# Performance work log

Measured on AMD Instinct MI355X. Metric: run time of the kernel, lower is better.

Reference implementation:

```python
import jax, jax.numpy as jnp
import numpy as np

E, D, F = 32, 2048, 768  # num_experts, hidden_size, intermediate_size
B, S, TOPK = 2, 1024, 8
T = B * S


def setup_inputs() -> dict:
    key = jax.random.key(0)
    k1, k2, k3, k4, k5 = jax.random.split(key, 5)
    hidden_states = jax.random.normal(k1, (B, S, D), dtype=jnp.float32)
    routing_weights = jax.random.uniform(k2, (T, E), dtype=jnp.float32)
    router_indices = jax.random.randint(k3, (T, TOPK), 0, E)
    gate_up_proj = jax.random.normal(k4, (E, D, 2 * F), dtype=jnp.float32) * 0.02
    down_proj = jax.random.normal(k5, (E, F, D), dtype=jnp.float32) * 0.02
    return {
        "hidden_states": hidden_states,
        "routing_weights": routing_weights,
        "router_indices": router_indices,
        "gate_up_proj": gate_up_proj,
        "down_proj": down_proj,
    }


def reference(hidden_states, routing_weights, router_indices, gate_up_proj, down_proj):
    batch_size = hidden_states.shape[0]
    x = hidden_states.reshape(-1, D)  # (T, D)
    gate_up = jnp.einsum('TD,EDF->TEF', x, gate_up_proj)  # (T, E, 2F)
    gate, up = jnp.split(gate_up, 2, axis=-1)
    gated = up * jax.nn.silu(gate)  # (T, E, F)
    next_states = jnp.einsum('TEF,EFD->TED', gated, down_proj)  # (T, E, D)
    next_states = (next_states * routing_weights[..., None]).sum(axis=1)  # (T, D)
    return next_states.reshape(batch_size, -1, D)
```

## Files before the change

kernel.cpp:

```cpp
#include <hip/hip_runtime.h>
#include <stdint.h>

#define NE 32
#define ND 2048
#define NF 768
#define NF2 1536
#define NT 2048
#define NEF (NE * NF)
#define KH 12288

#define BM 128
#define BN 64
#define BK 32
#define BSTR 40

typedef __attribute__((ext_vector_type(8))) short short8;
typedef __attribute__((ext_vector_type(4))) float floatx4;

__device__ __forceinline__ unsigned pk_bf16(float a, float b) {
  union { float f; unsigned u; } ua, ub;
  ua.f = a; ub.f = b;
  unsigned ra = (ua.u + 0x7fffu + ((ua.u >> 16) & 1u)) >> 16;
  unsigned rb = (ub.u + 0x7fffu + ((ub.u >> 16) & 1u)) & 0xffff0000u;
  return ra | rb;
}
__device__ __forceinline__ unsigned short bf16_1(float a) {
  union { float f; unsigned u; } ua; ua.f = a;
  return (unsigned short)((ua.u + 0x7fffu + ((ua.u >> 16) & 1u)) >> 16);
}

#define GLOAD_LDS16(g, l)                                                     \
  __builtin_amdgcn_global_load_lds(                                           \
      (const __attribute__((address_space(1))) void*)(g),                     \
      (__attribute__((address_space(3))) void*)(l), 16, 0, 0)

#define MF(a, b, c) __builtin_amdgcn_mfma_f32_16x16x32_bf16(a, b, c, 0, 0, 0)

__global__ void k_cvt_x(const float* __restrict__ x, unsigned short* __restrict__ xb, int n4) {
  int i = blockIdx.x * blockDim.x + threadIdx.x;
  if (i < n4) {
    float4 v = ((const float4*)x)[i];
    uint2 o;
    o.x = pk_bf16(v.x, v.y);
    o.y = pk_bf16(v.z, v.w);
    ((uint2*)xb)[i] = o;
  }
}

template <int PAIR>
__global__ void k_trans(const float* __restrict__ in, unsigned short* __restrict__ out,
                        int R, int C, size_t zstride) {
  __shared__ float sT[64][65];
  in  += (size_t)blockIdx.z * zstride;
  out += (size_t)blockIdx.z * zstride;
  const int r0 = blockIdx.y * 64, c0 = blockIdx.x * 64;
  const int t = threadIdx.x;
  const int lrow = t >> 4, lc4 = (t & 15) * 4;
#pragma unroll
  for (int i = 0; i < 4; i++) {
    float4 v = *(const float4*)&in[(size_t)(r0 + lrow + i * 16) * C + c0 + lc4];
    sT[lrow + i * 16][lc4 + 0] = v.x;
    sT[lrow + i * 16][lc4 + 1] = v.y;
    sT[lrow + i * 16][lc4 + 2] = v.z;
    sT[lrow + i * 16][lc4 + 3] = v.w;
  }
  __syncthreads();
  const int c = t >> 2, rg = (t & 3) * 16;
  uint4 o0, o1;
  o0.x = pk_bf16(sT[rg + 0][c],  sT[rg + 1][c]);
  o0.y = pk_bf16(sT[rg + 2][c],  sT[rg + 3][c]);
  o0.z = pk_bf16(sT[rg + 4][c],  sT[rg + 5][c]);
  o0.w = pk_bf16(sT[rg + 6][c],  sT[rg + 7][c]);
  o1.x = pk_bf16(sT[rg + 8][c],  sT[rg + 9][c]);
  o1.y = pk_bf16(sT[rg + 10][c], sT[rg + 11][c]);
  o1.z = pk_bf16(sT[rg + 12][c], sT[rg + 13][c]);
  o1.w = pk_bf16(sT[rg + 14][c], sT[rg + 15][c]);
  int oc = c0 + c;
  if (PAIR) {
    oc = (oc < NF) ? (((oc >> 5) << 6) + (oc & 31))
                   : ((((oc - NF) >> 5) << 6) + 32 + ((oc - NF) & 31));
  }
  unsigned short* op = &out[(size_t)oc * R + r0 + rg];
  ((uint4*)op)[0] = o0;
  ((uint4*)op)[1] = o1;
}

__global__ __launch_bounds__(512, 2) void k_gemm1p(
    const unsigned short* __restrict__ xb,
    const unsigned short* __restrict__ w1t,
    const float* __restrict__ rw,
    unsigned short* __restrict__ gws)
{
  __shared__ unsigned short sA[2][2][8192];
  __shared__ unsigned short sB[2][2][8192];
  __shared__ float srw[256];

  const int bx = blockIdx.x;
  const int L  = (bx & 7) * 192 + (bx >> 3);
  const int e  = L / 48;
  const int rem = L - e * 48;
  const int mt = rem & 7, nt = rem >> 3;
  const int m0 = mt * 256, n0 = nt * 256;

  const int tid = threadIdx.x;
  const int wid = tid >> 6, lane = tid & 63;
  const int wm2 = wid >> 2, wn4 = wid & 3;
  const int l15 = lane & 15, qg = lane >> 4;
  const int hb = wn4 >> 1, rbB = (wn4 & 1) * 64;

  if (tid < 256) srw[tid] = rw[(size_t)(m0 + tid) * NE + e];

  const int aoff0 = l15 * 64 + ((qg * 8) ^ ((l15 & 7) << 3));
  const int aoff1 = l15 * 64 + (((32 + qg * 8)) ^ ((l15 & 7) << 3));

  const int r8 = tid >> 3;
  const int csrc = ((tid & 7) ^ (r8 & 7)) * 8;
  const unsigned short* w1e = w1t + (size_t)e * NF2 * ND;
  const unsigned short* aSrc = xb  + (size_t)(m0 + r8) * ND + csrc;
  const unsigned short* bSrc = w1e + (size_t)(n0 + r8) * ND + csrc;

#define STAGE_A(buf, h, kt) do {                                              \
    const unsigned short* _g = aSrc + (size_t)(h) * 128 * ND + (size_t)(kt) * 64; \
    GLOAD_LDS16(_g, &sA[buf][h][wid * 512]);                                  \
    GLOAD_LDS16(_g + (size_t)64 * ND, &sA[buf][h][wid * 512 + 4096]);         \
  } while (0)
#define STAGE_B(buf, h, kt) do {                                              \
    const unsigned short* _g = bSrc + (size_t)(h) * 128 * ND + (size_t)(kt) * 64; \
    GLOAD_LDS16(_g, &sB[buf][h][wid * 512]);                                  \
    GLOAD_LDS16(_g + (size_t)64 * ND, &sB[buf][h][wid * 512 + 4096]);         \
  } while (0)

#define DS_A(buf, q) {                                                        \
    a0s0 = *(const short8*)&sA[buf][wm2][((q) * 32 +  0) * 64 + aoff0];       \
    a0s1 = *(const short8*)&sA[buf][wm2][((q) * 32 +  0) * 64 + aoff1];       \
    a1s0 = *(const short8*)&sA[buf][wm2][((q) * 32 + 16) * 64 + aoff0];       \
    a1s1 = *(const short8*)&sA[buf][wm2][((q) * 32 + 16) * 64 + aoff1];       \
  }
#define DS_B(buf) {                                                           \
    b0s0 = *(const short8*)&sB[buf][hb][(rbB +  0) * 64 + aoff0];             \
    b0s1 = *(const short8*)&sB[buf][hb][(rbB +  0) * 64 + aoff1];             \
    b1s0 = *(const short8*)&sB[buf][hb][(rbB + 16) * 64 + aoff0];             \
    b1s1 = *(const short8*)&sB[buf][hb][(rbB + 16) * 64 + aoff1];             \
    b2s0 = *(const short8*)&sB[buf][hb][(rbB + 32) * 64 + aoff0];             \
    b2s1 = *(const short8*)&sB[buf][hb][(rbB + 32) * 64 + aoff1];             \
    b3s0 = *(const short8*)&sB[buf][hb][(rbB + 48) * 64 + aoff0];             \
    b3s1 = *(const short8*)&sB[buf][hb][(rbB + 48) * 64 + aoff1];             \
  }
#define MM(q) do {                                                            \
    __builtin_amdgcn_s_setprio(1);                                            \
    acc[(q)*2+0][0] = MF(a0s0, b0s0, acc[(q)*2+0][0]);                        \
    acc[(q)*2+0][0] = MF(a0s1, b0s1, acc[(q)*2+0][0]);                        \
    acc[(q)*2+0][1] = MF(a0s0, b1s0, acc[(q)*2+0][1]);                        \
    acc[(q)*2+0][1] = MF(a0s1, b1s1, acc[(q)*2+0][1]);                        \
    acc[(q)*2+0][2] = MF(a0s0, b2s0, acc[(q)*2+0][2]);                        \
    acc[(q)*2+0][2] = MF(a0s1, b2s1, acc[(q)*2+0][2]);                        \
    acc[(q)*2+0][3] = MF(a0s0, b3s0, acc[(q)*2+0][3]);                        \
    acc[(q)*2+0][3] = MF(a0s1, b3s1, acc[(q)*2+0][3]);                        \
    acc[(q)*2+1][0] = MF(a1s0, b0s0, acc[(q)*2+1][0]);                        \
    acc[(q)*2+1][0] = MF(a1s1, b0s1, acc[(q)*2+1][0]);                        \
    acc[(q)*2+1][1] = MF(a1s0, b1s0, acc[(q)*2+1][1]);                        \
    acc[(q)*2+1][1] = MF(a1s1, b1s1, acc[(q)*2+1][1]);                        \
    acc[(q)*2+1][2] = MF(a1s0, b2s0, acc[(q)*2+1][2]);                        \
    acc[(q)*2+1][2] = MF(a1s1, b2s1, acc[(q)*2+1][2]);                        \
    acc[(q)*2+1][3] = MF(a1s0, b3s0, acc[(q)*2+1][3]);                        \
    acc[(q)*2+1][3] = MF(a1s1, b3s1, acc[(q)*2+1][3]);                        \
    __builtin_amdgcn_s_setprio(0);                                            \
  } while (0)

#define BAR_OPEN  asm volatile("s_barrier" ::: "memory")
#define BAR_CLOSE asm volatile("s_waitcnt lgkmcnt(0)\n\ts_barrier" ::: "memory")
#define VM4 asm volatile("s_waitcnt vmcnt(4)" ::: "memory")
#define VM0 asm volatile("s_waitcnt vmcnt(0)" ::: "memory")
#define S23_ON(x) x
#define S23_OFF(x)

#define KITER(t1, t2, t3, S23, VMT)                                           \
  DS_A(0, 0) DS_B(0) STAGE_A(1, 0, t1); BAR_OPEN; MM(0); BAR_CLOSE;           \
  DS_A(0, 1) STAGE_A(1, 1, t1); BAR_OPEN; MM(1); BAR_CLOSE;                   \
  DS_A(0, 2) S23(STAGE_B(0, 0, t2);) BAR_OPEN; MM(2); BAR_CLOSE;              \
  DS_A(0, 3) S23(STAGE_B(0, 1, t2);) VMT; BAR_OPEN; MM(3); BAR_CLOSE;         \
  DS_A(1, 0) DS_B(1) S23(STAGE_A(0, 0, t2);) BAR_OPEN; MM(0); BAR_CLOSE;      \
  DS_A(1, 1) S23(STAGE_A(0, 1, t2);) BAR_OPEN; MM(1); BAR_CLOSE;              \
  DS_A(1, 2) S23(STAGE_B(1, 0, t3);) BAR_OPEN; MM(2); BAR_CLOSE;              \
  DS_A(1, 3) S23(STAGE_B(1, 1, t3);) VMT; BAR_OPEN; MM(3); BAR_CLOSE;

  short8 a0s0, a0s1, a1s0, a1s1;
  short8 b0s0, b0s1, b1s0, b1s1, b2s0, b2s1, b3s0, b3s1;
  floatx4 acc[8][4];
#pragma unroll
  for (int i = 0; i < 8; i++)
#pragma unroll
    for (int j = 0; j < 4; j++) acc[i][j] = (floatx4){0.f, 0.f, 0.f, 0.f};

  STAGE_B(0, 0, 0); STAGE_B(0, 1, 0);
  STAGE_A(0, 0, 0); STAGE_A(0, 1, 0);
  STAGE_B(1, 0, 1); STAGE_B(1, 1, 1);
  VM4; BAR_OPEN;

  const int nI = ND / 64 / 2;
  for (int i = 0; i < nI - 1; ++i) {
    const int t1 = 2 * i + 1, t2 = 2 * i + 2, t3 = 2 * i + 3;
    KITER(t1, t2, t3, S23_ON, VM4)
  }
  {
    const int t1 = ND / 64 - 1;
    KITER(t1, 0, 0, S23_OFF, VM0)
  }

  const size_t cb = (size_t)e * NF + (size_t)nt * 128 + wn4 * 32 + l15;
#pragma unroll
  for (int mf = 0; mf < 8; ++mf) {
    const int rbase = wm2 * 128 + mf * 16 + qg * 4;
#pragma unroll
    for (int nf = 0; nf < 2; ++nf)
#pragma unroll
      for (int r = 0; r < 4; ++r) {
        float g = acc[mf][nf][r];
        float u = acc[mf][nf + 2][r];
        float sig = __builtin_amdgcn_rcpf(1.f + __expf(-g));
        float val = u * g * sig * srw[rbase + r];
        gws[(size_t)(m0 + rbase + r) * NEF + cb + nf * 16] = bf16_1(val);
      }
  }
#undef STAGE_A
#undef STAGE_B
#undef DS_A
#undef DS_B
#undef MM
#undef KITER
}

__global__ __launch_bounds__(256, 3) void k_gemm1b(
    const unsigned short* __restrict__ xb,
    const unsigned short* __restrict__ w1t,
    const float* __restrict__ rw,
    unsigned short* __restrict__ gws,
    int e0)
{
  __shared__ unsigned short sA[BM * BK];
  __shared__ unsigned short sG[BN * BK];
  __shared__ unsigned short sU[BN * BK];
  __shared__ float srw[BM];

  const int el  = blockIdx.y;
  const int e   = e0 + el;
  const int mt  = blockIdx.x & 15;
  const int nt  = blockIdx.x >> 4;
  const int m0  = mt * BM, n0 = nt * BN;
  const int tid = threadIdx.x;
  const int wid = tid >> 6, lane = tid & 63;
  const int wm = wid >> 1, wn = wid & 1;
  const int l15 = lane & 15, q = lane >> 4;

  if (tid < BM) srw[tid] = rw[(size_t)(m0 + tid) * NE + e];

  floatx4 accG[4][2], accU[4][2];
#pragma unroll
  for (int i = 0; i < 4; i++)
#pragma unroll
    for (int j = 0; j < 2; j++) {
      accG[i][j] = (floatx4){0.f, 0.f, 0.f, 0.f};
      accU[i][j] = (floatx4){0.f, 0.f, 0.f, 0.f};
    }

  const unsigned short* w1e = w1t + (size_t)el * NF2 * ND;

  const int koff = (lane & 3) * 8;
  const unsigned short* aptr = xb + (size_t)(m0 + wid * 32 + (lane >> 2)) * ND + koff;
  unsigned short* aLds = &sA[wid * 32 * BK];
  const unsigned short* gptr = w1e + (size_t)(n0 + wid * 16 + (lane >> 2)) * ND + koff;
  const unsigned short* uptr = gptr + (size_t)NF * ND;
  unsigned short* gLds = &sG[wid * 16 * BK];
  unsigned short* uLds = &sU[wid * 16 * BK];

  for (int kb = 0; kb < ND / BK; ++kb) {
    __syncthreads();
    GLOAD_LDS16(aptr + kb * BK, aLds);
    GLOAD_LDS16(aptr + kb * BK + 16 * ND, aLds + 16 * BK);
    GLOAD_LDS16(gptr + kb * BK, gLds);
    GLOAD_LDS16(uptr + kb * BK, uLds);
    __syncthreads();

    short8 bg0 = *(const short8*)&sG[(wn * 32 + 0  + l15) * BK + q * 8];
    short8 bg1 = *(const short8*)&sG[(wn * 32 + 16 + l15) * BK + q * 8];
    short8 bu0 = *(const short8*)&sU[(wn * 32 + 0  + l15) * BK + q * 8];
    short8 bu1 = *(const short8*)&sU[(wn * 32 + 16 + l15) * BK + q * 8];
#pragma unroll
    for (int i = 0; i < 4; i++) {
      short8 af = *(const short8*)&sA[(wm * 64 + i * 16 + l15) * BK + q * 8];
      accG[i][0] = MF(af, bg0, accG[i][0]);
      accG[i][1] = MF(af, bg1, accG[i][1]);
      accU[i][0] = MF(af, bu0, accU[i][0]);
      accU[i][1] = MF(af, bu1, accU[i][1]);
    }
  }

  const size_t obase = (size_t)m0 * NEF + (size_t)e * NF + n0 + wn * 32;
#pragma unroll
  for (int i = 0; i < 4; i++)
#pragma unroll
    for (int j = 0; j < 2; j++)
#pragma unroll
      for (int r = 0; r < 4; r++) {
        int row = wm * 64 + i * 16 + q * 4 + r;
        float g = accG[i][j][r];
        float u = accU[i][j][r];
        float sig = __builtin_amdgcn_rcpf(1.f + __expf(-g));
        float val = u * g * sig * srw[row];
        gws[obase + (size_t)row * NEF + j * 16 + l15] = bf16_1(val);
      }
}

template<int KSTRIDE, int HITERS>
__global__ __launch_bounds__(256, 3) void k_gemm2b(
    const unsigned short* __restrict__ gb,
    const unsigned short* __restrict__ w2t,
    float* __restrict__ out,
    int kbase)
{
  __shared__ unsigned short sA[BM * BK];
  __shared__ unsigned short sB[BN * BK];

  const int mt = blockIdx.x & 15;
  const int nt = blockIdx.x >> 4;
  const int m0 = mt * BM, n0 = nt * BN;
  const int tid = threadIdx.x;
  const int wid = tid >> 6, lane = tid & 63;
  const int wm = wid >> 1, wn = wid & 1;
  const int l15 = lane & 15, q = lane >> 4;

  const int kb0 = blockIdx.y * HITERS;
  const int kb1 = kb0 + HITERS;

  floatx4 acc[4][2];
#pragma unroll
  for (int i = 0; i < 4; i++)
#pragma unroll
    for (int j = 0; j < 2; j++) acc[i][j] = (floatx4){0.f, 0.f, 0.f, 0.f};

  const int koff = (lane & 3) * 8;
  const unsigned short* aptr = gb + (size_t)(m0 + wid * 32 + (lane >> 2)) * NEF + kbase + koff;
  unsigned short* aLds = &sA[wid * 32 * BK];
  const unsigned short* bptr = w2t + (size_t)(n0 + wid * 16 + (lane >> 2)) * KSTRIDE + koff;
  unsigned short* bLds = &sB[wid * 16 * BK];

  for (int kb = kb0; kb < kb1; ++kb) {
    __syncthreads();
    GLOAD_LDS16(aptr + kb * BK, aLds);
    GLOAD_LDS16(aptr + kb * BK + 16 * NEF, aLds + 16 * BK);
    GLOAD_LDS16(bptr + kb * BK, bLds);
    __syncthreads();

    short8 b0 = *(const short8*)&sB[(wn * 32 + 0  + l15) * BK + q * 8];
    short8 b1 = *(const short8*)&sB[(wn * 32 + 16 + l15) * BK + q * 8];
#pragma unroll
    for (int i = 0; i < 4; i++) {
      short8 af = *(const short8*)&sA[(wm * 64 + i * 16 + l15) * BK + q * 8];
      acc[i][0] = MF(af, b0, acc[i][0]);
      acc[i][1] = MF(af, b1, acc[i][1]);
    }
  }

#pragma unroll
  for (int i = 0; i < 4; i++)
#pragma unroll
    for (int j = 0; j < 2; j++)
#pragma unroll
      for (int r = 0; r < 4; r++) {
        int row = wm * 64 + i * 16 + q * 4 + r;
        unsafeAtomicAdd(&out[(size_t)(m0 + row) * ND + n0 + wn * 32 + j * 16 + l15],
                        acc[i][j][r]);
      }
}

__global__ __launch_bounds__(256, 2) void k_gemm1_legacy(
    const unsigned short* __restrict__ xb, const float* __restrict__ w1,
    const float* __restrict__ rw, unsigned short* __restrict__ gws)
{
  __shared__ unsigned short sA[BM * BK];
  __shared__ unsigned short sG[BN * BSTR];
  __shared__ unsigned short sU[BN * BSTR];
  __shared__ float srw[BM];
  const int e = blockIdx.y, mt = blockIdx.x & 15, nt = blockIdx.x >> 4;
  const int m0 = mt * BM, n0 = nt * BN;
  const int tid = threadIdx.x, wid = tid >> 6, lane = tid & 63;
  const int wm = wid >> 1, wn = wid & 1, l15 = lane & 15, q = lane >> 4;
  if (tid < BM) srw[tid] = rw[(size_t)(m0 + tid) * NE + e];
  const float* w1e = w1 + (size_t)e * ND * (2 * NF);
  floatx4 accG[4][2], accU[4][2];
#pragma unroll
  for (int i = 0; i < 4; i++)
#pragma unroll
    for (int j = 0; j < 2; j++) {
      accG[i][j] = (floatx4){0.f, 0.f, 0.f, 0.f};
      accU[i][j] = (floatx4){0.f, 0.f, 0.f, 0.f};
    }
  const int arow = wid * 32 + (lane >> 2), akoff = (lane & 3) * 8;
  const unsigned short* aptr = xb + (size_t)(m0 + arow) * ND + akoff;
  unsigned short* aLds = &sA[wid * 32 * BK];
  const float* gptr0 = w1e + (size_t)(wid * 8) * (2 * NF) + n0 + lane;
  for (int kb = 0; kb < ND / BK; ++kb) {
    const float* gp = gptr0 + (size_t)kb * BK * (2 * NF);
    float gv[8], uv[8];
#pragma unroll
    for (int r = 0; r < 8; r++) {
      gv[r] = gp[(size_t)r * (2 * NF)];
      uv[r] = gp[(size_t)r * (2 * NF) + NF];
    }
    __syncthreads();
    GLOAD_LDS16(aptr + kb * BK, aLds);
    GLOAD_LDS16(aptr + kb * BK + 16 * ND, aLds + 16 * BK);
    uint4 wg, wu;
    wg.x = pk_bf16(gv[0], gv[1]); wg.y = pk_bf16(gv[2], gv[3]);
    wg.z = pk_bf16(gv[4], gv[5]); wg.w = pk_bf16(gv[6], gv[7]);
    wu.x = pk_bf16(uv[0], uv[1]); wu.y = pk_bf16(uv[2], uv[3]);
    wu.z = pk_bf16(uv[4], uv[5]); wu.w = pk_bf16(uv[6], uv[7]);
    *((uint4*)&sG[lane * BSTR + wid * 8]) = wg;
    *((uint4*)&sU[lane * BSTR + wid * 8]) = wu;
    __syncthreads();
    short8 bg0 = *(const short8*)&sG[(wn * 32 + 0  + l15) * BSTR + q * 8];
    short8 bg1 = *(const short8*)&sG[(wn * 32 + 16 + l15) * BSTR + q * 8];
    short8 bu0 = *(const short8*)&sU[(wn * 32 + 0  + l15) * BSTR + q * 8];
    short8 bu1 = *(const short8*)&sU[(wn * 32 + 16 + l15) * BSTR + q * 8];
#pragma unroll
    for (int i = 0; i < 4; i++) {
      short8 af = *(const short8*)&sA[(wm * 64 + i * 16 + l15) * BK + q * 8];
      accG[i][0] = MF(af, bg0, accG[i][0]);
      accG[i][1] = MF(af, bg1, accG[i][1]);
      accU[i][0] = MF(af, bu0, accU[i][0]);
      accU[i][1] = MF(af, bu1, accU[i][1]);
    }
  }
  const size_t obase = (size_t)m0 * NEF + (size_t)e * NF + n0 + wn * 32;
#pragma unroll
  for (int i = 0; i < 4; i++)
#pragma unroll
    for (int j = 0; j < 2; j++)
#pragma unroll
      for (int r = 0; r < 4; r++) {
        int row = wm * 64 + i * 16 + q * 4 + r;
        float g = accG[i][j][r], u = accU[i][j][r];
        float sig = __builtin_amdgcn_rcpf(1.f + __expf(-g));
        gws[obase + (size_t)row * NEF + j * 16 + l15] = bf16_1(u * g * sig * srw[row]);
      }
}

__global__ __launch_bounds__(256, 2) void k_gemm2_legacy(
    const unsigned short* __restrict__ gb, const float* __restrict__ w2,
    float* __restrict__ out)
{
  __shared__ unsigned short sA[BM * BK];
  __shared__ unsigned short sB[BN * BSTR];
  const int mt = blockIdx.x & 15, nt = blockIdx.x >> 4;
  const int m0 = mt * BM, n0 = nt * BN;
  const int tid = threadIdx.x, wid = tid >> 6, lane = tid & 63;
  const int wm = wid >> 1, wn = wid & 1, l15 = lane & 15, q = lane >> 4;
  const int kb0 = blockIdx.y * (NEF / BK / 4), kb1 = kb0 + (NEF / BK / 4);
  floatx4 acc[4][2];
#pragma unroll
  for (int i = 0; i < 4; i++)
#pragma unroll
    for (int j = 0; j < 2; j++) acc[i][j] = (floatx4){0.f, 0.f, 0.f, 0.f};
  const int arow = wid * 32 + (lane >> 2), akoff = (lane & 3) * 8;
  const unsigned short* aptr = gb + (size_t)(m0 + arow) * NEF + akoff;
  unsigned short* aLds = &sA[wid * 32 * BK];
  const float* bptr0 = w2 + (size_t)(wid * 8) * ND + n0 + lane;
  for (int kb = kb0; kb < kb1; ++kb) {
    const float* bp = bptr0 + (size_t)kb * BK * ND;
    float bv[8];
#pragma unroll
    for (int r = 0; r < 8; r++) bv[r] = bp[(size_t)r * ND];
    __syncthreads();
    GLOAD_LDS16(aptr + kb * BK, aLds);
    GLOAD_LDS16(aptr + kb * BK + 16 * NEF, aLds + 16 * BK);
    uint4 wb;
    wb.x = pk_bf16(bv[0], bv[1]); wb.y = pk_bf16(bv[2], bv[3]);
    wb.z = pk_bf16(bv[4], bv[5]); wb.w = pk_bf16(bv[6], bv[7]);
    *((uint4*)&sB[lane * BSTR + wid * 8]) = wb;
    __syncthreads();
    short8 b0 = *(const short8*)&sB[(wn * 32 + 0  + l15) * BSTR + q * 8];
    short8 b1 = *(const short8*)&sB[(wn * 32 + 16 + l15) * BSTR + q * 8];
#pragma unroll
    for (int i = 0; i < 4; i++) {
      short8 af = *(const short8*)&sA[(wm * 64 + i * 16 + l15) * BK + q * 8];
      acc[i][0] = MF(af, b0, acc[i][0]);
      acc[i][1] = MF(af, b1, acc[i][1]);
    }
  }
#pragma unroll
  for (int i = 0; i < 4; i++)
#pragma unroll
    for (int j = 0; j < 2; j++)
#pragma unroll
      for (int r = 0; r < 4; r++) {
        int row = wm * 64 + i * 16 + q * 4 + r;
        unsafeAtomicAdd(&out[(size_t)(m0 + row) * ND + n0 + wn * 32 + j * 16 + l15],
                        acc[i][j][r]);
      }
}

extern "C" void kernel_launch(void* const* d_in, const int* in_sizes, int n_in,
                              void* d_out, int out_size, void* d_ws, size_t ws_size,
                              hipStream_t stream) {
  const float* x  = (const float*)d_in[0];
  const float* rw = (const float*)d_in[1];
  const float* w1 = (const float*)d_in[3];
  const float* w2 = (const float*)d_in[4];
  float* out = (float*)d_out;

  unsigned short* xb  = (unsigned short*)d_ws;
  unsigned short* gb  = xb + (size_t)NT * ND;
  unsigned short* wtb = gb + (size_t)NT * NEF;
  unsigned short* w1t = wtb;
  unsigned short* w2t = w1t + (size_t)NE * NF2 * ND;
  const size_t WS_FULL = ((size_t)NT * ND + (size_t)NT * NEF +
                          (size_t)NE * NF2 * ND + (size_t)ND * NEF) * 2;
  const size_t WS_NEED = ((size_t)NT * ND + (size_t)NT * NEF +
                          (size_t)8 * NF2 * ND) * 2;

  hipMemsetAsync(out, 0, (size_t)out_size * sizeof(float), stream);
  k_cvt_x<<<(NT * ND / 4 + 255) / 256, 256, 0, stream>>>(x, xb, NT * ND / 4);

  if (ws_size >= WS_FULL) {
    {
      dim3 gt(NF2 / 64, ND / 64, NE);
      k_trans<1><<<gt, 256, 0, stream>>>(w1, w1t, ND, NF2, (size_t)ND * NF2);
    }
    {
      dim3 gt(ND / 64, NEF / 64, 1);
      k_trans<0><<<gt, 256, 0, stream>>>(w2, w2t, NEF, ND, 0);
    }
    k_gemm1p<<<dim3(8 * 6 * NE), 512, 0, stream>>>(xb, w1t, rw, gb);
    {
      dim3 g2(16 * (ND / BN), 2);
      k_gemm2b<NEF, NEF / BK / 2><<<g2, 256, 0, stream>>>(gb, w2t, out, 0);
    }
  } else if (ws_size >= WS_NEED) {
    for (int qc = 0; qc < 4; ++qc) {
      dim3 gt(NF2 / 64, ND / 64, 8);
      k_trans<0><<<gt, 256, 0, stream>>>(w1 + (size_t)qc * 8 * ND * NF2, wtb,
                                         ND, NF2, (size_t)ND * NF2);
      dim3 g1(16 * (NF / BN), 8);
      k_gemm1b<<<g1, 256, 0, stream>>>(xb, wtb, rw, gb, qc * 8);
    }
    for (int h = 0; h < 2; ++h) {
      dim3 gt(ND / 64, KH / 64, 1);
      k_trans<0><<<gt, 256, 0, stream>>>(w2 + (size_t)h * KH * ND, wtb, KH, ND, 0);
      dim3 g2(16 * (ND / BN), 2);
      k_gemm2b<KH, KH / BK / 2><<<g2, 256, 0, stream>>>(gb, wtb, out, h * KH);
    }
  } else {
    dim3 gA(16 * (NF / BN), NE);
    k_gemm1_legacy<<<gA, 256, 0, stream>>>(xb, w1, rw, gb);
    dim3 gB(16 * (ND / BN), 4);
    k_gemm2_legacy<<<gB, 256, 0, stream>>>(gb, w2, out);
  }
}
```

Baseline: 1.426 ms.

## Replace second GEMM with 256x256-tile pipelined split-K kernel using LDS direct loads

Adds k_gemm2p, a 512-thread kernel that computes the down-projection GEMM with 256x256 output tiles, a 4-way split over the K dimension and double-buffered global-to-LDS loads. It reuses the same swizzled pipeline machinery as the first GEMM, with a block-index remap for locality. Partial results are accumulated into the output with atomic adds. It replaces the older 128x64 split-2 kernel in the full-workspace path. The goal is more data reuse per tile and better latency hiding, at the cost of more atomic traffic and only 256 blocks.

```diff
diff --git a/kernel.cpp b/kernel.cpp
--- a/kernel.cpp
+++ b/kernel.cpp
@@ -224,10 +224,100 @@
   }
 #undef STAGE_A
 #undef STAGE_B
+#undef KITER
+}
+
+__global__ __launch_bounds__(512, 2) void k_gemm2p(
+    const unsigned short* __restrict__ gb,
+    const unsigned short* __restrict__ w2t,
+    float* __restrict__ out)
+{
+  __shared__ unsigned short sA[2][2][8192];
+  __shared__ unsigned short sB[2][2][8192];
+
+  const int bx = blockIdx.x;
+  const int L  = (bx & 7) * 32 + (bx >> 3);
+  const int ks = L & 3;
+  const int tile = L >> 2;
+  const int mt = tile & 7, nt = tile >> 3;
+  const int m0 = mt * 256, n0 = nt * 256;
+
+  const int tid = threadIdx.x;
+  const int wid = tid >> 6, lane = tid & 63;
+  const int wm2 = wid >> 2, wn4 = wid & 3;
+  const int l15 = lane & 15, qg = lane >> 4;
+  const int hb = wn4 >> 1, rbB = (wn4 & 1) * 64;
+
+  const int aoff0 = l15 * 64 + ((qg * 8) ^ ((l15 & 7) << 3));
+  const int aoff1 = l15 * 64 + (((32 + qg * 8)) ^ ((l15 & 7) << 3));
+
+  const int r8 = tid >> 3;
+  const int csrc = ((tid & 7) ^ (r8 & 7)) * 8;
+  const size_t kb0e = (size_t)ks * (NEF / 4);
+  const unsigned short* aSrc = gb  + (size_t)(m0 + r8) * NEF + kb0e + csrc;
+  const unsigned short* bSrc = w2t + (size_t)(n0 + r8) * NEF + kb0e + csrc;
+
+#define STAGE2_A(buf, h, kt) do {                                             \
+    const unsigned short* _g = aSrc + (size_t)(h) * 128 * NEF + (size_t)(kt) * 64; \
+    GLOAD_LDS16(_g, &sA[buf][h][wid * 512]);                                  \
+    GLOAD_LDS16(_g + (size_t)64 * NEF, &sA[buf][h][wid * 512 + 4096]);        \
+  } while (0)
+#define STAGE2_B(buf, h, kt) do {                                             \
+    const unsigned short* _g = bSrc + (size_t)(h) * 128 * NEF + (size_t)(kt) * 64; \
+    GLOAD_LDS16(_g, &sB[buf][h][wid * 512]);                                  \
+    GLOAD_LDS16(_g + (size_t)64 * NEF, &sB[buf][h][wid * 512 + 4096]);        \
+  } while (0)
+
+#define KITER2(t1, t2, t3, S23, VMT)                                          \
+  DS_A(0, 0) DS_B(0) STAGE2_A(1, 0, t1); BAR_OPEN; MM(0); BAR_CLOSE;          \
+  DS_A(0, 1) STAGE2_A(1, 1, t1); BAR_OPEN; MM(1); BAR_CLOSE;                  \
+  DS_A(0, 2) S23(STAGE2_B(0, 0, t2);) BAR_OPEN; MM(2); BAR_CLOSE;             \
+  DS_A(0, 3) S23(STAGE2_B(0, 1, t2);) VMT; BAR_OPEN; MM(3); BAR_CLOSE;        \
+  DS_A(1, 0) DS_B(1) S23(STAGE2_A(0, 0, t2);) BAR_OPEN; MM(0); BAR_CLOSE;     \
+  DS_A(1, 1) S23(STAGE2_A(0, 1, t2);) BAR_OPEN; MM(1); BAR_CLOSE;             \
+  DS_A(1, 2) S23(STAGE2_B(1, 0, t3);) BAR_OPEN; MM(2); BAR_CLOSE;             \
+  DS_A(1, 3) S23(STAGE2_B(1, 1, t3);) VMT; BAR_OPEN; MM(3); BAR_CLOSE;
+
+  short8 a0s0, a0s1, a1s0, a1s1;
+  short8 b0s0, b0s1, b1s0, b1s1, b2s0, b2s1, b3s0, b3s1;
+  floatx4 acc[8][4];
+#pragma unroll
+  for (int i = 0; i < 8; i++)
+#pragma unroll
+    for (int j = 0; j < 4; j++) acc[i][j] = (floatx4){0.f, 0.f, 0.f, 0.f};
+
+  STAGE2_B(0, 0, 0); STAGE2_B(0, 1, 0);
+  STAGE2_A(0, 0, 0); STAGE2_A(0, 1, 0);
+  STAGE2_B(1, 0, 1); STAGE2_B(1, 1, 1);
+  VM4; BAR_OPEN;
+
+  const int nI = (NEF / 4) / 64 / 2;
+  for (int i = 0; i < nI - 1; ++i) {
+    const int t1 = 2 * i + 1, t2 = 2 * i + 2, t3 = 2 * i + 3;
+    KITER2(t1, t2, t3, S23_ON, VM4)
+  }
+  {
+    const int t1 = (NEF / 4) / 64 - 1;
+    KITER2(t1, 0, 0, S23_OFF, VM0)
+  }
+
+#pragma unroll
+  for (int mf = 0; mf < 8; ++mf) {
+    const int row = m0 + wm2 * 128 + mf * 16 + qg * 4;
+#pragma unroll
+    for (int nf = 0; nf < 4; ++nf) {
+      const int col = n0 + hb * 128 + rbB + nf * 16 + l15;
+#pragma unroll
+      for (int r = 0; r < 4; ++r)
+        unsafeAtomicAdd(&out[(size_t)(row + r) * ND + col], acc[mf][nf][r]);
+    }
+  }
+#undef STAGE2_A
+#undef STAGE2_B
+#undef KITER2
 #undef DS_A
 #undef DS_B
 #undef MM
-#undef KITER
 }
 
 __global__ __launch_bounds__(256, 3) void k_gemm1b(
@@ -531,10 +621,7 @@
       k_trans<0><<<gt, 256, 0, stream>>>(w2, w2t, NEF, ND, 0);
     }
     k_gemm1p<<<dim3(8 * 6 * NE), 512, 0, stream>>>(xb, w1t, rw, gb);
-    {
-      dim3 g2(16 * (ND / BN), 2);
-      k_gemm2b<NEF, NEF / BK / 2><<<g2, 256, 0, stream>>>(gb, w2t, out, 0);
-    }
+    k_gemm2p<<<dim3(256), 512, 0, stream>>>(gb, w2t, out);
   } else if (ws_size >= WS_NEED) {
     for (int qc = 0; qc < 4; ++qc) {
       dim3 gt(NF2 / 64, ND / 64, 8);
```

Result: faster. 1.326 ms (-7.0%).
